# Kernel optimization log

Measured on AMD Instinct MI355X. Metric: run time of the kernel, lower is better.

Reference implementation:

```python
import jax, jax.numpy as jnp
import numpy as np

EMB_SIZE = 50000
D = 256            # emb_dimension
TIMES = 3
D3 = D * TIMES     # 768
RESCALE = 20.0
BATCH = 128
NEG = 5


def setup_inputs() -> dict:
    key = jax.random.key(0)
    ks = jax.random.split(key, 12)
    initrange = 1.0 / D
    return {
        "pos_u": jax.random.randint(ks[0], (BATCH,), 0, EMB_SIZE),
        "pos_v": jax.random.randint(ks[1], (BATCH,), 0, EMB_SIZE),
        "neg_v": jax.random.randint(ks[2], (BATCH, NEG), 0, EMB_SIZE),
        "time": jax.random.uniform(ks[3], (BATCH,), dtype=jnp.float32) * RESCALE,
        "m1": jax.random.normal(ks[4], (1, D), dtype=jnp.float32) / jnp.sqrt(2.0),
        "b1": jax.random.normal(ks[5], (D,), dtype=jnp.float32) * 0.5,
        "W2": jax.random.normal(ks[6], (D, D), dtype=jnp.float32) / jnp.sqrt(D),   # dense2 weight (out,in)
        "b2": jnp.zeros((D,), dtype=jnp.float32),
        "W4": jax.random.normal(ks[7], (D3, D), dtype=jnp.float32) / jnp.sqrt(D),  # dense4 weight (out,in)
        "b4": jnp.zeros((D3,), dtype=jnp.float32),
        "U": jax.random.uniform(ks[8], (EMB_SIZE, D3), dtype=jnp.float32,
                                 minval=-initrange, maxval=initrange),
        "V": jax.random.uniform(ks[9], (EMB_SIZE, D3), dtype=jnp.float32,
                                 minval=-initrange, maxval=initrange),
        "T": jax.random.normal(ks[10], (D, D, D3), dtype=jnp.float32) / D,
        "B": jax.random.normal(ks[11], (D, D), dtype=jnp.float32) / D,
    }


def reference(pos_u, pos_v, neg_v, time, m1, b1, W2, b2, W4, b4, U, V, T, B):
    # time encoding: h1 = tanh(t/rescale * m1 + b1); timevec = tanh(dense2(h1))
    h1 = jnp.tanh((time[:, None] / RESCALE) * m1 + b1)          # (b, d)
    tv = jnp.tanh(h1 @ W2.T + b2)                               # (b, d)
    tvB = tv @ B                                                # einsum('bij,bi->bj') of broadcast B

    # positive target word: (T . emb_u + B) contracted with timevec, then dense4
    emb_u = U[pos_u]                                            # (b, 3d)
    h3_u = jnp.einsum('ijk,bk,bi->bj', T, emb_u, tv) + tvB      # (b, d)
    use_w = h3_u @ W4.T + b4                                    # (b, 3d)

    # positive context word
    emb_v = V[pos_v]                                            # (b, 3d)
    h3_v = jnp.einsum('ijk,bk,bi->bj', T, emb_v, tv) + tvB      # (b, d)
    use_c_v = h3_v @ W4.T + b4                                  # (b, 3d)

    # negative samples: fused contraction avoids the (b, l, d, d) intermediate
    emb_n = V[neg_v]                                            # (b, l, 3d)
    h3_n = jnp.einsum('ijk,blk,bi->blj', T, emb_n, tv) + tvB[:, None, :]  # (b, l, d)
    use_c_n = h3_n @ W4.T + b4                                  # (b, l, 3d)

    score = jnp.sum(use_w * use_c_v, axis=1)
    score = jnp.clip(score, -10.0, 10.0)
    score = -jax.nn.log_sigmoid(score)                          # (b,)

    neg_score = jnp.einsum('blk,bk->bl', use_c_n, use_w)        # bmm with use_w
    neg_score = jnp.clip(neg_score, -10.0, 10.0)
    neg_score = -jnp.mean(jax.nn.log_sigmoid(-neg_score), axis=1)  # (b,)

    return (jnp.mean(score + neg_score), jnp.mean(score), jnp.mean(neg_score))
```

## Files before the change

kernel.cpp:

```cpp
#include <hip/hip_runtime.h>
#include <hip/hip_bf16.h>

#define DD   256
#define DD3  768
#define NB   128
#define NE   7

#define OFF_TVT  0u
#define OFF_TVB  32768u
#define OFF_EMB  65536u
#define OFF_H3   753664u
#define OFF_G    983040u
#define OFF_GV   1048576u
#define OFF_SC   1048832u

typedef __attribute__((ext_vector_type(8))) short bf16x8;
typedef __attribute__((ext_vector_type(4))) float f32x4;

__device__ __forceinline__ unsigned bf16rne(float f) {
  unsigned u = __float_as_uint(f);
  return (u + 0x7fffu + ((u >> 16) & 1u)) >> 16;
}

__device__ __forceinline__ void gld16(const float* g, float* l) {
  __builtin_amdgcn_global_load_lds(
      (const __attribute__((address_space(1))) unsigned int*)g,
      (__attribute__((address_space(3))) unsigned int*)l, 16, 0, 0);
}

__global__ void k_setup(const float* __restrict__ timev,
                        const float* __restrict__ m1,
                        const float* __restrict__ b1,
                        const float* __restrict__ W2,
                        const float* __restrict__ b2,
                        const float* __restrict__ Bm,
                        float* __restrict__ tv_t,
                        float* __restrict__ tvB) {
  const int b = blockIdx.x, i = threadIdx.x;
  __shared__ float h1[DD];
  __shared__ float tvs[DD];
  const float t = timev[b] * (1.0f / 20.0f);
  h1[i] = tanhf(fmaf(t, m1[i], b1[i]));
  __syncthreads();
  float acc = b2[i];
  const float* w2r = W2 + i * DD;
#pragma unroll 8
  for (int jj = 0; jj < DD; ++jj) acc = fmaf(h1[jj], w2r[jj], acc);
  const float tvi = tanhf(acc);
  tvs[i] = tvi;
  tv_t[i * NB + b] = tvi;
  __syncthreads();
  float a2 = 0.f;
#pragma unroll 8
  for (int ii = 0; ii < DD; ++ii) a2 = fmaf(tvs[ii], Bm[ii * DD + i], a2);
  tvB[b * DD + i] = a2;
}

__global__ void k_pack(const float* __restrict__ tv_t, short* __restrict__ tvf) {
  const int t = blockIdx.x * 256 + threadIdx.x;
  const int f = t >> 6, l = t & 63;
  const int b = (f >> 3) * 16 + (l & 15);
  const int i0 = (f & 7) * 32 + ((l >> 4) & 3) * 8;
  bf16x8 v;
#pragma unroll
  for (int jj = 0; jj < 8; ++jj)
    v[jj] = (short)bf16rne(tv_t[(i0 + jj) * NB + b]);
  *(bf16x8*)(tvf + (long)t * 8) = v;
}

__global__ void k_gather(const int* __restrict__ pos_u,
                         const int* __restrict__ pos_v,
                         const int* __restrict__ neg_v,
                         const float* __restrict__ U,
                         const float* __restrict__ V,
                         float* __restrict__ emb) {
  const int be = blockIdx.x;
  const int b = be / NE, e = be % NE;
  const float* src;
  if (e == 0)      src = U + (long)pos_u[b] * DD3;
  else if (e == 1) src = V + (long)pos_v[b] * DD3;
  else             src = V + (long)neg_v[b * 5 + (e - 2)] * DD3;
  const float4 v = ((const float4*)src)[threadIdx.x];
  ((float4*)(emb + ((long)e * NB + b) * DD3))[threadIdx.x] = v;
}

__global__ __launch_bounds__(1024) void k_gram(const float* __restrict__ W4,
                                               const float* __restrict__ b4,
                                               float* __restrict__ G,
                                               float* __restrict__ gv) {
  const int p = blockIdx.x, t = threadIdx.x;
  const int q = t & 255, nq = t >> 8;
  __shared__ float colp[DD3];
  __shared__ float red[4][257];
  __shared__ float gred[4];
  for (int n = t; n < DD3; n += 1024) colp[n] = W4[n * DD + p];
  __syncthreads();
  float acc = 0.f;
  const int n0 = nq * 192;
#pragma unroll 8
  for (int n = n0; n < n0 + 192; ++n) acc = fmaf(colp[n], W4[n * DD + q], acc);
  red[nq][q] = acc;
  float gp = 0.f;
  for (int n = n0; n < n0 + 192; ++n) gp = fmaf(b4[n], colp[n], gp);
  if (q == 0) gred[nq] = gp;
  __syncthreads();
  if (t < 256) G[p * DD + t] = red[0][t] + red[1][t] + red[2][t] + red[3][t];
  if (t == 0) gv[p] = gred[0] + gred[1] + gred[2] + gred[3];
}

__global__ __launch_bounds__(512, 4) void k_main(const float* __restrict__ T,
                                                 const short* __restrict__ tvf,
                                                 const float* __restrict__ emb,
                                                 const float* __restrict__ tvB,
                                                 float* __restrict__ h3) {
  __shared__ float Ts[3][4096];
  __shared__ float h3red[NB][NE];
  const int bid = blockIdx.x;
  const int j = bid & 255;
  const int kc = bid >> 8;

  const int t = threadIdx.x;
  const int l = t & 63;
  const int w = t >> 6;
  const int bq = w >> 1;
  const int mh = w & 1;
  const int l15 = l & 15;
  const int l4 = (l >> 4) & 3;
  const int lhi = l >> 5;
  const int kb = (l & 31) * 4;

  bf16x8 tvfr[2][8];
#pragma unroll
  for (int nf = 0; nf < 2; ++nf)
#pragma unroll
    for (int it = 0; it < 8; ++it)
      tvfr[nf][it] = *(const bf16x8*)(tvf + ((((bq * 2 + nf) * 8) + it) * 64 + l) * 8);

  const int i0 = 4 * w + lhi, i1 = i0 + 2;
  const float* gp0 = T + (long)i0 * 196608 + j * 768 + kc * 128 + (kb ^ (((i0 >> 3) & 3) << 4));
  const float* gp1 = T + (long)i1 * 196608 + j * 768 + kc * 128 + (kb ^ (((i1 >> 3) & 3) << 4));

  auto stage = [&](int it) {
    const int buf = it % 3;
    const long o = (long)it * 6291456;
    gld16(gp0 + o, &Ts[buf][(w * 2 + 0) * 256]);
    gld16(gp1 + o, &Ts[buf][(w * 2 + 1) * 256]);
  };

  const int kcol0 = mh * 64;

  f32x4 acc[4][2];
#pragma unroll
  for (int mf = 0; mf < 4; ++mf) {
    acc[mf][0] = {0.f, 0.f, 0.f, 0.f};
    acc[mf][1] = {0.f, 0.f, 0.f, 0.f};
  }

  stage(0); stage(1);

#pragma unroll
  for (int it = 0; it < 8; ++it) {
    if (it < 6) {
      stage(it + 2);
      asm volatile("s_waitcnt vmcnt(4)" ::: "memory");
    } else if (it == 6) {
      asm volatile("s_waitcnt vmcnt(2)" ::: "memory");
    } else {
      asm volatile("s_waitcnt vmcnt(0)" ::: "memory");
    }
    __builtin_amdgcn_s_barrier();
    asm volatile("" ::: "memory");
    const float* tsb = &Ts[it % 3][0];
    __builtin_amdgcn_s_setprio(1);
#pragma unroll
    for (int mf = 0; mf < 4; ++mf) {
      const int kx = (kcol0 + mf * 16 + l15) ^ (l4 << 4);
      bf16x8 af;
#pragma unroll
      for (int jj = 0; jj < 8; ++jj)
        af[jj] = (short)bf16rne(tsb[(l4 * 8 + jj) * 128 + kx]);
      acc[mf][0] = __builtin_amdgcn_mfma_f32_16x16x32_bf16(af, tvfr[0][it], acc[mf][0], 0, 0, 0);
      acc[mf][1] = __builtin_amdgcn_mfma_f32_16x16x32_bf16(af, tvfr[1][it], acc[mf][1], 0, 0, 0);
    }
    __builtin_amdgcn_s_setprio(0);
    asm volatile("" ::: "memory");
    __builtin_amdgcn_s_barrier();
    asm volatile("" ::: "memory");
  }

  float h3p[NE][2];
#pragma unroll
  for (int e = 0; e < NE; ++e) { h3p[e][0] = 0.f; h3p[e][1] = 0.f; }
#pragma unroll
  for (int nf = 0; nf < 2; ++nf) {
    const int b = bq * 32 + nf * 16 + l15;
#pragma unroll
    for (int mf = 0; mf < 4; ++mf) {
      const long ko = (long)kc * 128 + mh * 64 + mf * 16 + l4 * 4;
#pragma unroll
      for (int e = 0; e < NE; ++e) {
        const f32x4 em = *(const f32x4*)(emb + ((long)e * NB + b) * 768 + ko);
        float s = h3p[e][nf];
        s = fmaf(acc[mf][nf][0], em[0], s);
        s = fmaf(acc[mf][nf][1], em[1], s);
        s = fmaf(acc[mf][nf][2], em[2], s);
        s = fmaf(acc[mf][nf][3], em[3], s);
        h3p[e][nf] = s;
      }
    }
  }

  float hr[NE][2];
#pragma unroll
  for (int e = 0; e < NE; ++e)
#pragma unroll
    for (int nf = 0; nf < 2; ++nf) {
      float v = h3p[e][nf];
      v += __shfl_xor(v, 16);
      v += __shfl_xor(v, 32);
      hr[e][nf] = v;
    }
  __syncthreads();
  if (mh == 0 && l < 16) {
#pragma unroll
    for (int e = 0; e < NE; ++e) {
      h3red[bq * 32 + l][e]      = hr[e][0];
      h3red[bq * 32 + 16 + l][e] = hr[e][1];
    }
  }
  __syncthreads();
  if (mh == 1 && l < 16) {
#pragma unroll
    for (int nf = 0; nf < 2; ++nf) {
      const int b = bq * 32 + nf * 16 + l;
      const float tb = (kc == 0) ? tvB[b * DD + j] : 0.f;
#pragma unroll
      for (int e = 0; e < NE; ++e)
        atomicAdd(&h3[((long)b * NE + e) * DD + j], h3red[b][e] + hr[e][nf] + tb);
    }
  }
}

__global__ void k_score(const float* __restrict__ h3,
                        const float* __restrict__ G,
                        const float* __restrict__ gv,
                        const float* __restrict__ b4,
                        float* __restrict__ scoreb,
                        float* __restrict__ negb) {
  const int b = blockIdx.x, t = threadIdx.x;
  __shared__ float h3s[NE * DD];
  __shared__ float red[4][16];
  for (int idx = t; idx < NE * DD; idx += 256) h3s[idx] = h3[(long)b * NE * DD + idx];
  __syncthreads();
  float racc = 0.f;
#pragma unroll 8
  for (int jp = 0; jp < DD; ++jp) racc = fmaf(G[jp * DD + t], h3s[jp], racc);

  float loc[14];
#pragma unroll
  for (int e = 1; e < NE; ++e) loc[e - 1] = racc * h3s[e * DD + t];
  loc[6] = gv[t] * h3s[t];
#pragma unroll
  for (int e = 1; e < NE; ++e) loc[6 + e] = gv[t] * h3s[e * DD + t];
  loc[13] = b4[t] * b4[t] + b4[t + 256] * b4[t + 256] + b4[t + 512] * b4[t + 512];

  const int lane = t & 63, wid = t >> 6;
#pragma unroll
  for (int qd = 0; qd < 14; ++qd) {
    float v = loc[qd];
#pragma unroll
    for (int m = 1; m < 64; m <<= 1) v += __shfl_xor(v, m);
    if (lane == 0) red[wid][qd] = v;
  }
  __syncthreads();
  if (t == 0) {
    float r[14];
#pragma unroll
    for (int qd = 0; qd < 14; ++qd)
      r[qd] = red[0][qd] + red[1][qd] + red[2][qd] + red[3][qd];
    const float c = r[13], gu = r[6];
    auto logsig = [](float x) { return fminf(x, 0.f) - log1pf(expf(-fabsf(x))); };
    float dv = r[0] + gu + r[7] + c;
    dv = fminf(fmaxf(dv, -10.f), 10.f);
    const float sc = -logsig(dv);
    float ns = 0.f;
    for (int lx = 1; lx < 6; ++lx) {
      float dn = r[lx] + gu + r[7 + lx] + c;
      dn = fminf(fmaxf(dn, -10.f), 10.f);
      ns -= logsig(-dn);
    }
    scoreb[b] = sc;
    negb[b] = ns * 0.2f;
  }
}

__global__ void k_final(const float* __restrict__ scoreb,
                        const float* __restrict__ negb,
                        float* __restrict__ out) {
  const int t = threadIdx.x;
  float s = scoreb[t], n = negb[t];
#pragma unroll
  for (int m = 1; m < 64; m <<= 1) {
    s += __shfl_xor(s, m);
    n += __shfl_xor(n, m);
  }
  __shared__ float rs[2], rn[2];
  if ((t & 63) == 0) { rs[t >> 6] = s; rn[t >> 6] = n; }
  __syncthreads();
  if (t == 0) {
    const float S = (rs[0] + rs[1]) * (1.0f / 128.0f);
    const float N = (rn[0] + rn[1]) * (1.0f / 128.0f);
    out[0] = S + N;
    out[1] = S;
    out[2] = N;
  }
}

extern "C" void kernel_launch(void* const* d_in, const int* in_sizes, int n_in,
                              void* d_out, int out_size, void* d_ws, size_t ws_size,
                              hipStream_t stream) {
  const int*   pos_u = (const int*)d_in[0];
  const int*   pos_v = (const int*)d_in[1];
  const int*   neg_v = (const int*)d_in[2];
  const float* timev = (const float*)d_in[3];
  const float* m1    = (const float*)d_in[4];
  const float* b1    = (const float*)d_in[5];
  const float* W2    = (const float*)d_in[6];
  const float* b2    = (const float*)d_in[7];
  const float* W4    = (const float*)d_in[8];
  const float* b4    = (const float*)d_in[9];
  const float* U     = (const float*)d_in[10];
  const float* V     = (const float*)d_in[11];
  const float* T     = (const float*)d_in[12];
  const float* Bm    = (const float*)d_in[13];

  float* ws     = (float*)d_ws;
  float* tv_t   = ws + OFF_TVT;
  float* tvB    = ws + OFF_TVB;
  float* emb    = ws + OFF_EMB;
  float* h3     = ws + OFF_H3;
  float* G      = ws + OFF_G;
  float* gv     = ws + OFF_GV;
  short* tvf    = (short*)(ws + OFF_SC);
  float* scoreb = ws + OFF_SC;
  float* negb   = ws + OFF_SC + 128;
  float* out    = (float*)d_out;

  hipMemsetAsync(h3, 0, (size_t)NB * NE * DD * sizeof(float), stream);
  k_setup<<<128, 256, 0, stream>>>(timev, m1, b1, W2, b2, Bm, tv_t, tvB);
  k_pack<<<16, 256, 0, stream>>>(tv_t, tvf);
  k_gather<<<896, 192, 0, stream>>>(pos_u, pos_v, neg_v, U, V, emb);
  k_gram<<<256, 1024, 0, stream>>>(W4, b4, G, gv);
  k_main<<<1536, 512, 0, stream>>>(T, tvf, emb, tvB, h3);
  k_score<<<128, 256, 0, stream>>>(h3, G, gv, b4, scoreb, negb);
  k_final<<<1, 128, 0, stream>>>(scoreb, negb, out);
}
```

Before: 205.5 us.

## Repack T into bf16 MFMA fragment layout before the main contraction

Adds a kernel that converts the fp32 T tensor to bf16 and lays it out in the exact MFMA A-fragment order. A new main kernel then loads fragments straight from global memory with register double-buffering, skipping the LDS staging, the barriers and the in-loop conversion. The goal is to simplify the inner loop and halve the bytes the contraction reads. In exchange, every call now does an extra full pass over T: it reads the fp32 tensor and writes a bf16 copy, which needs a large workspace. If the workspace is too small, the code falls back to the old kernel.

```diff
diff --git a/kernel.cpp b/kernel.cpp
--- a/kernel.cpp
+++ b/kernel.cpp
@@ -13,6 +13,8 @@
 #define OFF_G    983040u
 #define OFF_GV   1048576u
 #define OFF_SC   1048832u
+#define OFF_TF   1065216u
+
 
 typedef __attribute__((ext_vector_type(8))) short bf16x8;
 typedef __attribute__((ext_vector_type(4))) float f32x4;
@@ -108,6 +110,162 @@
   if (t == 0) gv[p] = gred[0] + gred[1] + gred[2] + gred[3];
 }
 
+__global__ __launch_bounds__(512) void k_repack(const float* __restrict__ T,
+                                                short* __restrict__ Tf) {
+  __shared__ float Ls[16 * 772];
+  const int it = blockIdx.x >> 7;
+  const int jp = blockIdx.x & 127;
+  const int j0 = jp * 2;
+  const int t = threadIdx.x;
+  const int w = t >> 6, lane = t & 63;
+
+#pragma unroll 1
+  for (int l4 = 0; l4 < 4; ++l4) {
+    const int i = it * 32 + l4 * 8 + w;
+    float4 v[2][3];
+#pragma unroll
+    for (int jl = 0; jl < 2; ++jl) {
+      const float4* src = (const float4*)(T + (long)i * 196608 + (j0 + jl) * 768);
+#pragma unroll
+      for (int c = 0; c < 3; ++c) v[jl][c] = src[c * 64 + lane];
+    }
+#pragma unroll
+    for (int jl = 0; jl < 2; ++jl) {
+      const int row = w * 2 + jl;
+#pragma unroll
+      for (int c = 0; c < 3; ++c)
+        *(float4*)&Ls[row * 772 + (c * 64 + lane) * 4] = v[jl][c];
+    }
+    __syncthreads();
+#pragma unroll
+    for (int q = 0; q < 3; ++q) {
+      const int F = t + 512 * q;
+      const int l15 = F & 15;
+      const int mf = (F >> 4) & 3;
+      const int mh = (F >> 6) & 1;
+      const int jc = F >> 7;
+      const int kc = jc % 6;
+      const int jl = jc / 6;
+      const int k = kc * 128 + mh * 64 + mf * 16 + l15;
+      bf16x8 o;
+#pragma unroll
+      for (int jj = 0; jj < 8; ++jj)
+        o[jj] = (short)bf16rne(Ls[(jj * 2 + jl) * 772 + k]);
+      const long FI = (long)(j0 + jl) * 24576 + kc * 4096 + it * 512 +
+                      mh * 256 + mf * 64 + l4 * 16 + l15;
+      *(bf16x8*)(Tf + FI * 8) = o;
+    }
+    __syncthreads();
+  }
+}
+
+__global__ __launch_bounds__(512) void k_main_f(const short* __restrict__ Tf,
+                                                const short* __restrict__ tvf,
+                                                const float* __restrict__ emb,
+                                                const float* __restrict__ tvB,
+                                                float* __restrict__ h3) {
+  __shared__ float h3red[NB][NE];
+  const int bid = blockIdx.x;
+  const int j = bid & 255;
+  const int kc = bid >> 8;
+
+  const int t = threadIdx.x;
+  const int l = t & 63;
+  const int w = t >> 6;
+  const int bq = w >> 1;
+  const int mh = w & 1;
+  const int l15 = l & 15;
+  const int l4 = (l >> 4) & 3;
+
+  bf16x8 tvfr[2][8];
+#pragma unroll
+  for (int nf = 0; nf < 2; ++nf)
+#pragma unroll
+    for (int it = 0; it < 8; ++it)
+      tvfr[nf][it] = *(const bf16x8*)(tvf + ((((bq * 2 + nf) * 8) + it) * 64 + l) * 8);
+
+  const bf16x8* fr = (const bf16x8*)Tf + ((long)j * 24576 + kc * 4096 + mh * 256 + l);
+
+  f32x4 acc[4][2];
+#pragma unroll
+  for (int mf = 0; mf < 4; ++mf) {
+    acc[mf][0] = {0.f, 0.f, 0.f, 0.f};
+    acc[mf][1] = {0.f, 0.f, 0.f, 0.f};
+  }
+
+  bf16x8 afb[2][4];
+#pragma unroll
+  for (int mf = 0; mf < 4; ++mf) afb[0][mf] = fr[mf * 64];
+
+#pragma unroll
+  for (int it = 0; it < 8; ++it) {
+    if (it < 7) {
+#pragma unroll
+      for (int mf = 0; mf < 4; ++mf)
+        afb[(it + 1) & 1][mf] = fr[(it + 1) * 512 + mf * 64];
+    }
+    __builtin_amdgcn_s_setprio(1);
+#pragma unroll
+    for (int mf = 0; mf < 4; ++mf) {
+      acc[mf][0] = __builtin_amdgcn_mfma_f32_16x16x32_bf16(afb[it & 1][mf], tvfr[0][it], acc[mf][0], 0, 0, 0);
+      acc[mf][1] = __builtin_amdgcn_mfma_f32_16x16x32_bf16(afb[it & 1][mf], tvfr[1][it], acc[mf][1], 0, 0, 0);
+    }
+    __builtin_amdgcn_s_setprio(0);
+  }
+
+  float h3p[NE][2];
+#pragma unroll
+  for (int e = 0; e < NE; ++e) { h3p[e][0] = 0.f; h3p[e][1] = 0.f; }
+#pragma unroll
+  for (int nf = 0; nf < 2; ++nf) {
+    const int b = bq * 32 + nf * 16 + l15;
+#pragma unroll
+    for (int mf = 0; mf < 4; ++mf) {
+      const long ko = (long)kc * 128 + mh * 64 + mf * 16 + l4 * 4;
+#pragma unroll
+      for (int e = 0; e < NE; ++e) {
+        const f32x4 em = *(const f32x4*)(emb + ((long)e * NB + b) * 768 + ko);
+        float s = h3p[e][nf];
+        s = fmaf(acc[mf][nf][0], em[0], s);
+        s = fmaf(acc[mf][nf][1], em[1], s);
+        s = fmaf(acc[mf][nf][2], em[2], s);
+        s = fmaf(acc[mf][nf][3], em[3], s);
+        h3p[e][nf] = s;
+      }
+    }
+  }
+
+  float hr[NE][2];
+#pragma unroll
+  for (int e = 0; e < NE; ++e)
+#pragma unroll
+    for (int nf = 0; nf < 2; ++nf) {
+      float v = h3p[e][nf];
+      v += __shfl_xor(v, 16);
+      v += __shfl_xor(v, 32);
+      hr[e][nf] = v;
+    }
+  __syncthreads();
+  if (mh == 0 && l < 16) {
+#pragma unroll
+    for (int e = 0; e < NE; ++e) {
+      h3red[bq * 32 + l][e]      = hr[e][0];
+      h3red[bq * 32 + 16 + l][e] = hr[e][1];
+    }
+  }
+  __syncthreads();
+  if (mh == 1 && l < 16) {
+#pragma unroll
+    for (int nf = 0; nf < 2; ++nf) {
+      const int b = bq * 32 + nf * 16 + l;
+      const float tb = (kc == 0) ? tvB[b * DD + j] : 0.f;
+#pragma unroll
+      for (int e = 0; e < NE; ++e)
+        atomicAdd(&h3[((long)b * NE + e) * DD + j], h3red[b][e] + hr[e][nf] + tb);
+    }
+  }
+}
+
 __global__ __launch_bounds__(512, 4) void k_main(const float* __restrict__ T,
                                                  const short* __restrict__ tvf,
                                                  const float* __restrict__ emb,
@@ -148,7 +306,6 @@
   };
 
   const int kcol0 = mh * 64;
-
   f32x4 acc[4][2];
 #pragma unroll
   for (int mf = 0; mf < 4; ++mf) {
@@ -157,7 +314,6 @@
   }
 
   stage(0); stage(1);
-
 #pragma unroll
   for (int it = 0; it < 8; ++it) {
     if (it < 6) {
@@ -342,16 +498,24 @@
   float* G      = ws + OFF_G;
   float* gv     = ws + OFF_GV;
   short* tvf    = (short*)(ws + OFF_SC);
+  short* Tf     = (short*)(ws + OFF_TF);
   float* scoreb = ws + OFF_SC;
   float* negb   = ws + OFF_SC + 128;
   float* out    = (float*)d_out;
+
+  const size_t need = (size_t)OFF_TF * 4 + (size_t)6291456 * 16;
 
   hipMemsetAsync(h3, 0, (size_t)NB * NE * DD * sizeof(float), stream);
   k_setup<<<128, 256, 0, stream>>>(timev, m1, b1, W2, b2, Bm, tv_t, tvB);
   k_pack<<<16, 256, 0, stream>>>(tv_t, tvf);
   k_gather<<<896, 192, 0, stream>>>(pos_u, pos_v, neg_v, U, V, emb);
   k_gram<<<256, 1024, 0, stream>>>(W4, b4, G, gv);
-  k_main<<<1536, 512, 0, stream>>>(T, tvf, emb, tvB, h3);
+  if (ws_size >= need) {
+    k_repack<<<1024, 512, 0, stream>>>(T, Tf);
+    k_main_f<<<1536, 512, 0, stream>>>(Tf, tvf, emb, tvB, h3);
+  } else {
+    k_main<<<1536, 512, 0, stream>>>(T, tvf, emb, tvB, h3);
+  }
   k_score<<<128, 256, 0, stream>>>(h3, G, gv, b4, scoreb, negb);
   k_final<<<1, 128, 0, stream>>>(scoreb, negb, out);
 }
```

New measurement: 260.4 us. 26.7% more time.

## Pre-repack T into bf16 MFMA fragment layout and transpose gathered embeddings

Applied to the files above, without the earlier changes.

Adds a kernel that converts the fp32 T tensor into bf16 stored directly in MFMA fragment order, so the main kernel loads fragments straight to registers with double buffering instead of staging through LDS with barriers. Embedding gather now writes a transposed layout to make the epilogue loads coalesced. The repack runs every call, adding a full extra read of T plus a half-size write and reread, trading more HBM traffic for a simpler, barrier-free main loop.

```diff
diff --git a/kernel.cpp b/kernel.cpp
--- a/kernel.cpp
+++ b/kernel.cpp
@@ -8,11 +8,13 @@
 
 #define OFF_TVT  0u
 #define OFF_TVB  32768u
-#define OFF_EMB  65536u
+#define OFF_EMBT 65536u
 #define OFF_H3   753664u
 #define OFF_G    983040u
 #define OFF_GV   1048576u
 #define OFF_SC   1048832u
+#define OFF_TF   1065216u
+
 
 typedef __attribute__((ext_vector_type(8))) short bf16x8;
 typedef __attribute__((ext_vector_type(4))) float f32x4;
@@ -20,12 +22,6 @@
 __device__ __forceinline__ unsigned bf16rne(float f) {
   unsigned u = __float_as_uint(f);
   return (u + 0x7fffu + ((u >> 16) & 1u)) >> 16;
-}
-
-__device__ __forceinline__ void gld16(const float* g, float* l) {
-  __builtin_amdgcn_global_load_lds(
-      (const __attribute__((address_space(1))) unsigned int*)g,
-      (__attribute__((address_space(3))) unsigned int*)l, 16, 0, 0);
 }
 
 __global__ void k_setup(const float* __restrict__ timev,
@@ -68,20 +64,42 @@
   *(bf16x8*)(tvf + (long)t * 8) = v;
 }
 
-__global__ void k_gather(const int* __restrict__ pos_u,
-                         const int* __restrict__ pos_v,
-                         const int* __restrict__ neg_v,
-                         const float* __restrict__ U,
-                         const float* __restrict__ V,
-                         float* __restrict__ emb) {
-  const int be = blockIdx.x;
-  const int b = be / NE, e = be % NE;
-  const float* src;
-  if (e == 0)      src = U + (long)pos_u[b] * DD3;
-  else if (e == 1) src = V + (long)pos_v[b] * DD3;
-  else             src = V + (long)neg_v[b * 5 + (e - 2)] * DD3;
-  const float4 v = ((const float4*)src)[threadIdx.x];
-  ((float4*)(emb + ((long)e * NB + b) * DD3))[threadIdx.x] = v;
+__global__ __launch_bounds__(256) void k_embT(const int* __restrict__ pos_u,
+                                              const int* __restrict__ pos_v,
+                                              const int* __restrict__ neg_v,
+                                              const float* __restrict__ U,
+                                              const float* __restrict__ V,
+                                              float* __restrict__ embT) {
+  __shared__ float Ls[64 * 133];
+  const int e = blockIdx.x / 12, kt = blockIdx.x % 12;
+  const int t = threadIdx.x;
+#pragma unroll 1
+  for (int rep = 0; rep < 8; ++rep) {
+    const int idx = rep * 256 + t;
+    const int b = idx >> 4, f4 = idx & 15;
+    int row;
+    if (e == 0)      row = pos_u[b];
+    else if (e == 1) row = pos_v[b];
+    else             row = neg_v[b * 5 + (e - 2)];
+    const float* src = (e == 0) ? U : V;
+    const float4 v = *(const float4*)(src + (long)row * DD3 + kt * 64 + f4 * 4);
+    Ls[(f4 * 4 + 0) * 133 + b] = v.x;
+    Ls[(f4 * 4 + 1) * 133 + b] = v.y;
+    Ls[(f4 * 4 + 2) * 133 + b] = v.z;
+    Ls[(f4 * 4 + 3) * 133 + b] = v.w;
+  }
+  __syncthreads();
+#pragma unroll 1
+  for (int rep = 0; rep < 8; ++rep) {
+    const int idx = rep * 256 + t;
+    const int k = idx >> 5, fb = idx & 31;
+    float4 o;
+    o.x = Ls[k * 133 + fb * 4 + 0];
+    o.y = Ls[k * 133 + fb * 4 + 1];
+    o.z = Ls[k * 133 + fb * 4 + 2];
+    o.w = Ls[k * 133 + fb * 4 + 3];
+    *(float4*)(embT + ((long)e * DD3 + kt * 64 + k) * NB + fb * 4) = o;
+  }
 }
 
 __global__ __launch_bounds__(1024) void k_gram(const float* __restrict__ W4,
@@ -108,12 +126,60 @@
   if (t == 0) gv[p] = gred[0] + gred[1] + gred[2] + gred[3];
 }
 
-__global__ __launch_bounds__(512, 4) void k_main(const float* __restrict__ T,
-                                                 const short* __restrict__ tvf,
-                                                 const float* __restrict__ emb,
-                                                 const float* __restrict__ tvB,
-                                                 float* __restrict__ h3) {
-  __shared__ float Ts[3][4096];
+__global__ __launch_bounds__(512) void k_repack(const float* __restrict__ T,
+                                                short* __restrict__ Tf) {
+  __shared__ float Ls[16 * 772];
+  const int it = blockIdx.x >> 7;
+  const int jp = blockIdx.x & 127;
+  const int j0 = jp * 2;
+  const int t = threadIdx.x;
+  const int w = t >> 6, lane = t & 63;
+
+#pragma unroll 1
+  for (int l4 = 0; l4 < 4; ++l4) {
+    const int i = it * 32 + l4 * 8 + w;
+    float4 v[2][3];
+#pragma unroll
+    for (int jl = 0; jl < 2; ++jl) {
+      const float4* src = (const float4*)(T + (long)i * 196608 + (j0 + jl) * 768);
+#pragma unroll
+      for (int c = 0; c < 3; ++c) v[jl][c] = src[c * 64 + lane];
+    }
+#pragma unroll
+    for (int jl = 0; jl < 2; ++jl) {
+      const int row = w * 2 + jl;
+#pragma unroll
+      for (int c = 0; c < 3; ++c)
+        *(float4*)&Ls[row * 772 + (c * 64 + lane) * 4] = v[jl][c];
+    }
+    __syncthreads();
+#pragma unroll
+    for (int q = 0; q < 3; ++q) {
+      const int F = t + 512 * q;
+      const int l15 = F & 15;
+      const int mf = (F >> 4) & 3;
+      const int mh = (F >> 6) & 1;
+      const int jc = F >> 7;
+      const int kc = jc % 6;
+      const int jl = jc / 6;
+      const int k = kc * 128 + mh * 64 + mf * 16 + l15;
+      bf16x8 o;
+#pragma unroll
+      for (int jj = 0; jj < 8; ++jj)
+        o[jj] = (short)bf16rne(Ls[(jj * 2 + jl) * 772 + k]);
+      const long FI = (long)(j0 + jl) * 24576 + kc * 4096 + it * 512 +
+                      mh * 256 + mf * 64 + l4 * 16 + l15;
+      *(bf16x8*)(Tf + FI * 8) = o;
+    }
+    __syncthreads();
+  }
+}
+
+__global__ __launch_bounds__(512, 3) void k_main_f(const short* __restrict__ Tf,
+                                                   const short* __restrict__ tvf,
+                                                   const float* __restrict__ embT,
+                                                   const float* __restrict__ tvB,
+                                                   float* __restrict__ h3) {
   __shared__ float h3red[NB][NE];
   const int bid = blockIdx.x;
   const int j = bid & 255;
@@ -126,28 +192,9 @@
   const int mh = w & 1;
   const int l15 = l & 15;
   const int l4 = (l >> 4) & 3;
-  const int lhi = l >> 5;
-  const int kb = (l & 31) * 4;
-
-  bf16x8 tvfr[2][8];
-#pragma unroll
-  for (int nf = 0; nf < 2; ++nf)
-#pragma unroll
-    for (int it = 0; it < 8; ++it)
-      tvfr[nf][it] = *(const bf16x8*)(tvf + ((((bq * 2 + nf) * 8) + it) * 64 + l) * 8);
-
-  const int i0 = 4 * w + lhi, i1 = i0 + 2;
-  const float* gp0 = T + (long)i0 * 196608 + j * 768 + kc * 128 + (kb ^ (((i0 >> 3) & 3) << 4));
-  const float* gp1 = T + (long)i1 * 196608 + j * 768 + kc * 128 + (kb ^ (((i1 >> 3) & 3) << 4));
-
-  auto stage = [&](int it) {
-    const int buf = it % 3;
-    const long o = (long)it * 6291456;
-    gld16(gp0 + o, &Ts[buf][(w * 2 + 0) * 256]);
-    gld16(gp1 + o, &Ts[buf][(w * 2 + 1) * 256]);
-  };
-
-  const int kcol0 = mh * 64;
+
+  const bf16x8* fr  = (const bf16x8*)Tf + ((long)j * 24576 + kc * 4096 + mh * 256 + l);
+  const bf16x8* tvp = (const bf16x8*)tvf + l;
 
   f32x4 acc[4][2];
 #pragma unroll
@@ -156,56 +203,49 @@
     acc[mf][1] = {0.f, 0.f, 0.f, 0.f};
   }
 
-  stage(0); stage(1);
+  bf16x8 afb[2][4];
+  bf16x8 tvb[2][2];
+#pragma unroll
+  for (int mf = 0; mf < 4; ++mf) afb[0][mf] = fr[mf * 64];
+#pragma unroll
+  for (int nf = 0; nf < 2; ++nf) tvb[0][nf] = tvp[((bq * 2 + nf) * 8) * 64];
 
 #pragma unroll
   for (int it = 0; it < 8; ++it) {
-    if (it < 6) {
-      stage(it + 2);
-      asm volatile("s_waitcnt vmcnt(4)" ::: "memory");
-    } else if (it == 6) {
-      asm volatile("s_waitcnt vmcnt(2)" ::: "memory");
-    } else {
-      asm volatile("s_waitcnt vmcnt(0)" ::: "memory");
-    }
-    __builtin_amdgcn_s_barrier();
-    asm volatile("" ::: "memory");
-    const float* tsb = &Ts[it % 3][0];
-    __builtin_amdgcn_s_setprio(1);
+    const int cur = it & 1, nxt = cur ^ 1;
+    if (it < 7) {
+#pragma unroll
+      for (int mf = 0; mf < 4; ++mf) afb[nxt][mf] = fr[(it + 1) * 512 + mf * 64];
+#pragma unroll
+      for (int nf = 0; nf < 2; ++nf) tvb[nxt][nf] = tvp[((bq * 2 + nf) * 8 + it + 1) * 64];
+    }
 #pragma unroll
     for (int mf = 0; mf < 4; ++mf) {
-      const int kx = (kcol0 + mf * 16 + l15) ^ (l4 << 4);
-      bf16x8 af;
-#pragma unroll
-      for (int jj = 0; jj < 8; ++jj)
-        af[jj] = (short)bf16rne(tsb[(l4 * 8 + jj) * 128 + kx]);
-      acc[mf][0] = __builtin_amdgcn_mfma_f32_16x16x32_bf16(af, tvfr[0][it], acc[mf][0], 0, 0, 0);
-      acc[mf][1] = __builtin_amdgcn_mfma_f32_16x16x32_bf16(af, tvfr[1][it], acc[mf][1], 0, 0, 0);
-    }
-    __builtin_amdgcn_s_setprio(0);
-    asm volatile("" ::: "memory");
-    __builtin_amdgcn_s_barrier();
-    asm volatile("" ::: "memory");
+      acc[mf][0] = __builtin_amdgcn_mfma_f32_16x16x32_bf16(afb[cur][mf], tvb[cur][0], acc[mf][0], 0, 0, 0);
+      acc[mf][1] = __builtin_amdgcn_mfma_f32_16x16x32_bf16(afb[cur][mf], tvb[cur][1], acc[mf][1], 0, 0, 0);
+    }
   }
 
   float h3p[NE][2];
 #pragma unroll
   for (int e = 0; e < NE; ++e) { h3p[e][0] = 0.f; h3p[e][1] = 0.f; }
-#pragma unroll
-  for (int nf = 0; nf < 2; ++nf) {
-    const int b = bq * 32 + nf * 16 + l15;
-#pragma unroll
-    for (int mf = 0; mf < 4; ++mf) {
-      const long ko = (long)kc * 128 + mh * 64 + mf * 16 + l4 * 4;
+
+  const float* et = embT + (long)(kc * 128 + mh * 64 + l4 * 4) * NB + bq * 32 + l15;
+#pragma unroll
+  for (int mf = 0; mf < 4; ++mf) {
+#pragma unroll
+    for (int q = 0; q < 4; ++q) {
+      const int kro = (mf * 16 + q) * NB;
+      float v[NE][2];
 #pragma unroll
       for (int e = 0; e < NE; ++e) {
-        const f32x4 em = *(const f32x4*)(emb + ((long)e * NB + b) * 768 + ko);
-        float s = h3p[e][nf];
-        s = fmaf(acc[mf][nf][0], em[0], s);
-        s = fmaf(acc[mf][nf][1], em[1], s);
-        s = fmaf(acc[mf][nf][2], em[2], s);
-        s = fmaf(acc[mf][nf][3], em[3], s);
-        h3p[e][nf] = s;
+        v[e][0] = et[(long)e * 98304 + kro];
+        v[e][1] = et[(long)e * 98304 + kro + 16];
+      }
+#pragma unroll
+      for (int e = 0; e < NE; ++e) {
+        h3p[e][0] = fmaf(acc[mf][0][q], v[e][0], h3p[e][0]);
+        h3p[e][1] = fmaf(acc[mf][1][q], v[e][1], h3p[e][1]);
       }
     }
   }
@@ -337,11 +377,12 @@
   float* ws     = (float*)d_ws;
   float* tv_t   = ws + OFF_TVT;
   float* tvB    = ws + OFF_TVB;
-  float* emb    = ws + OFF_EMB;
+  float* embT   = ws + OFF_EMBT;
   float* h3     = ws + OFF_H3;
   float* G      = ws + OFF_G;
   float* gv     = ws + OFF_GV;
   short* tvf    = (short*)(ws + OFF_SC);
+  short* Tf     = (short*)(ws + OFF_TF);
   float* scoreb = ws + OFF_SC;
   float* negb   = ws + OFF_SC + 128;
   float* out    = (float*)d_out;
@@ -349,9 +390,10 @@
   hipMemsetAsync(h3, 0, (size_t)NB * NE * DD * sizeof(float), stream);
   k_setup<<<128, 256, 0, stream>>>(timev, m1, b1, W2, b2, Bm, tv_t, tvB);
   k_pack<<<16, 256, 0, stream>>>(tv_t, tvf);
-  k_gather<<<896, 192, 0, stream>>>(pos_u, pos_v, neg_v, U, V, emb);
+  k_embT<<<84, 256, 0, stream>>>(pos_u, pos_v, neg_v, U, V, embT);
   k_gram<<<256, 1024, 0, stream>>>(W4, b4, G, gv);
-  k_main<<<1536, 512, 0, stream>>>(T, tvf, emb, tvB, h3);
+  k_repack<<<1024, 512, 0, stream>>>(T, Tf);
+  k_main_f<<<1536, 512, 0, stream>>>(Tf, tvf, embT, tvB, h3);
   k_score<<<128, 256, 0, stream>>>(h3, G, gv, b4, scoreb, negb);
   k_final<<<1, 128, 0, stream>>>(scoreb, negb, out);
 }
```

New measurement: 235.6 us. +14.7%, slower.
